# Performance work log

Hardware: AMD Instinct MI355X
Metric: run time of the kernel (lower is better)

## Reference

```python
import jax, jax.numpy as jnp
import numpy as np

B, TOPN, OUT, PAD, IOU_TH, IM = 16, 4, 224, 224, 0.25, 448
HP = IM + 2 * PAD  # padded image side = 896

_ANCHOR_SETTINGS = (
    dict(stride=32, size=48, scale=[2 ** (1. / 3.), 2 ** (2. / 3.)], aspect_ratio=[0.667, 1, 1.5]),
    dict(stride=64, size=96, scale=[2 ** (1. / 3.), 2 ** (2. / 3.)], aspect_ratio=[0.667, 1, 1.5]),
    dict(stride=128, size=192, scale=[1, 2 ** (1. / 3.), 2 ** (2. / 3.)], aspect_ratio=[0.667, 1, 1.5]),
)

def _edge_anchors(input_shape=(IM, IM)):
    # NTS-Net generate_default_anchor_maps: per layer, loop scale then aspect,
    # each emitting an HxW map flattened row-major -> matches tidy conv channel-major flatten.
    out = []
    for a in _ANCHOR_SETTINGS:
        st = a['stride']
        H = int(np.ceil(input_shape[0] / st)); W = int(np.ceil(input_shape[1] / st))
        cy = np.broadcast_to((np.arange(H) * st + st / 2.)[:, None], (H, W))
        cx = np.broadcast_to((np.arange(W) * st + st / 2.)[None, :], (H, W))
        for sc in a['scale']:
            for ar in a['aspect_ratio']:
                h = a['size'] * sc / np.sqrt(ar); w = a['size'] * sc * np.sqrt(ar)
                out.append(np.stack([cy - h / 2., cx - w / 2., cy + h / 2., cx + w / 2.], -1).reshape(-1, 4))
    e = np.concatenate(out, 0)
    return (e + PAD).astype(np.int32)  # module does (edge_anchors + 224).astype(int)


def _conv(x, w, b, stride, pad):
    y = jax.lax.conv_general_dilated(x, w, (stride, stride), [(pad, pad), (pad, pad)],
                                     dimension_numbers=('NCHW', 'OIHW', 'NCHW'))
    return y + b[None, :, None, None]


def _proposal_scores(rpn, w1, b1, w2, b2, w3, b3, wt1, bt1, wt2, bt2, wt3, bt3):
    d1 = jax.nn.relu(_conv(rpn, w1, b1, 1, 1))   # [B,128,14,14]
    d2 = jax.nn.relu(_conv(d1, w2, b2, 2, 1))    # [B,128,7,7]
    d3 = jax.nn.relu(_conv(d2, w3, b3, 2, 1))    # [B,128,4,4]
    bsz = rpn.shape[0]
    t1 = _conv(d1, wt1, bt1, 1, 0).reshape(bsz, -1)  # [B,1176]
    t2 = _conv(d2, wt2, bt2, 1, 0).reshape(bsz, -1)  # [B,294]
    t3 = _conv(d3, wt3, bt3, 1, 0).reshape(bsz, -1)  # [B,144]
    return jnp.concatenate([t1, t2, t3], axis=1)     # [B,1614]


def _nms_topn(scores, boxes, areas):
    # greedy hard NMS, fixed TOPN picks, suppress iou >= IOU_TH (matches upstream hard_nms)
    def step(s, _):
        i = jnp.argmax(s)
        sb = boxes[i]
        iy = jnp.clip(jnp.minimum(boxes[:, 2], sb[2]) - jnp.maximum(boxes[:, 0], sb[0]), 0.)
        ix = jnp.clip(jnp.minimum(boxes[:, 3], sb[3]) - jnp.maximum(boxes[:, 1], sb[1]), 0.)
        inter = iy * ix
        iou = inter / (areas + areas[i] - inter)
        return jnp.where(iou >= IOU_TH, -jnp.inf, s), i
    _, idxs = jax.lax.scan(step, scores, None, length=TOPN)
    return idxs  # [TOPN] int


def _crop_resize(x, anchors, top_idx):
    # batched replacement of the per-(i,j) F.interpolate(x_pad[i,:,y0:y1,x0:x1], 224, bilinear, align_corners=True)
    x_pad = jnp.pad(x, ((0, 0), (0, 0), (PAD, PAD), (PAD, PAD)))
    xp = jnp.transpose(x_pad, (0, 2, 3, 1))            # [B,HP,HP,3]
    bxs = anchors[top_idx].astype(jnp.float32)          # [B,T,4] (y0,x0,y1,x1)
    y0, x0, y1, x1 = bxs[..., 0], bxs[..., 1], bxs[..., 2], bxs[..., 3]
    t = jnp.arange(OUT, dtype=jnp.float32) / (OUT - 1)  # align_corners=True grid
    ys = y0[..., None] + t * (y1 - y0 - 1.)[..., None]  # [B,T,S] src rows in padded img
    xs = x0[..., None] + t * (x1 - x0 - 1.)[..., None]
    yi0 = jnp.floor(ys).astype(jnp.int32); yi1 = jnp.minimum(yi0 + 1, HP - 1)
    xi0 = jnp.floor(xs).astype(jnp.int32); xi1 = jnp.minimum(xi0 + 1, HP - 1)
    wy = (ys - yi0)[..., :, None, None]                 # [B,T,S,1,1]
    wx = (xs - xi0)[..., None, :, None]                 # [B,T,1,S,1]
    b = jnp.arange(x.shape[0])[:, None, None, None]
    g = lambda yi, xi: xp[b, yi[..., :, None], xi[..., None, :]]  # [B,T,S,S,3]
    v = (g(yi0, xi0) * (1 - wy) * (1 - wx) + g(yi0, xi1) * (1 - wy) * wx
         + g(yi1, xi0) * wy * (1 - wx) + g(yi1, xi1) * wy * wx)
    return jnp.transpose(v, (0, 1, 4, 2, 3))            # [B,T,3,S,S]


def setup_inputs() -> dict:
    key = jax.random.key(0)
    ks = jax.random.split(key, 16)
    he = lambda k, shape, fan: jax.random.normal(k, shape, jnp.float32) * np.sqrt(2.0 / fan)
    inp = {
        'x': jax.random.normal(ks[0], (B, 3, IM, IM), jnp.float32),
        'rpn_feature': jax.random.uniform(ks[1], (B, 2048, 14, 14), jnp.float32),
        'w_down1': he(ks[2], (128, 2048, 3, 3), 2048 * 9), 'b_down1': jnp.zeros((128,), jnp.float32),
        'w_down2': he(ks[3], (128, 128, 3, 3), 128 * 9),   'b_down2': jnp.zeros((128,), jnp.float32),
        'w_down3': he(ks[4], (128, 128, 3, 3), 128 * 9),   'b_down3': jnp.zeros((128,), jnp.float32),
        'w_tidy1': he(ks[5], (6, 128, 1, 1), 128),         'b_tidy1': jnp.zeros((6,), jnp.float32),
        'w_tidy2': he(ks[6], (6, 128, 1, 1), 128),         'b_tidy2': jnp.zeros((6,), jnp.float32),
        'w_tidy3': he(ks[7], (9, 128, 1, 1), 128),         'b_tidy3': jnp.zeros((9,), jnp.float32),
        'anchors': jnp.asarray(_edge_anchors(), jnp.int32),  # [1614,4]
    }
    return inp


def reference(x, rpn_feature, w_down1, b_down1, w_down2, b_down2, w_down3, b_down3,
              w_tidy1, b_tidy1, w_tidy2, b_tidy2, w_tidy3, b_tidy3, anchors):
    rpn_score = _proposal_scores(rpn_feature, w_down1, b_down1, w_down2, b_down2, w_down3, b_down3,
                                 w_tidy1, b_tidy1, w_tidy2, b_tidy2, w_tidy3, b_tidy3)
    boxes = anchors.astype(jnp.float32)
    areas = (boxes[:, 2] - boxes[:, 0]) * (boxes[:, 3] - boxes[:, 1])
    top_idx = jax.vmap(lambda s: _nms_topn(s, boxes, areas))(rpn_score)       # [B,TOPN]
    top_prob = jnp.take_along_axis(rpn_score, top_idx, axis=1)                # [B,TOPN]
    part_imgs = _crop_resize(x, anchors, top_idx).reshape(B * TOPN, 3, OUT, OUT)
    return part_imgs, top_idx, top_prob, rpn_score
```

## Files before the change

kernel.cpp:

```cpp
#include <hip/hip_runtime.h>
#include <math.h>

#define BATCH 16
#define TOPN 4
#define OUTS 224
#define PADW 224
#define IM 448
#define HP 896
#define NA 1614
#define IC1 2048
#define C128 128

#define N_PART (BATCH*TOPN*3*OUTS*OUTS)
#define OFF_TOPIDX  (N_PART)
#define OFF_TOPPROB (N_PART + BATCH*TOPN)
#define OFF_SCORE   (N_PART + 2*BATCH*TOPN)

#define WS_D1 0
#define WS_IDX (BATCH*C128*196)
#define WS_WT  (WS_IDX + 64)
#define NWT1 (9*2048*128)
#define NWT2 (9*128*128)
#define NIMG (16*32*16384)

typedef __attribute__((ext_vector_type(8))) short frag8;
typedef __attribute__((ext_vector_type(16))) float acc16;
typedef __attribute__((ext_vector_type(4)))  float acc4;

__device__ __forceinline__ unsigned short f2bf(float f) {
    unsigned int u = __float_as_uint(f);
    u = (u + 0x7fffu + ((u >> 16) & 1u)) >> 16;
    return (unsigned short)u;
}
__device__ __forceinline__ float bf2f(unsigned short h) {
    return __uint_as_float(((unsigned int)h) << 16);
}
__device__ __forceinline__ void cvt4(const float* v, ushort4* h, ushort4* lo) {
    unsigned short hh[4], ll[4];
#pragma unroll
    for (int e = 0; e < 4; ++e) { hh[e] = f2bf(v[e]); ll[e] = f2bf(v[e] - bf2f(hh[e])); }
    *h  = make_ushort4(hh[0], hh[1], hh[2], hh[3]);
    *lo = make_ushort4(ll[0], ll[1], ll[2], ll[3]);
}

__device__ __forceinline__ void wrepack_body(const float* __restrict__ w,
                                             unsigned short* __restrict__ w_hi,
                                             unsigned short* __restrict__ w_lo,
                                             int IC, int i) {
    if (i >= 128 * IC) return;
    int oc = i / IC, ic = i % IC;
    const float* src = w + (size_t)(oc * IC + ic) * 9;
#pragma unroll
    for (int tap = 0; tap < 9; ++tap) {
        float v = src[tap];
        unsigned short h = f2bf(v);
        size_t gi = ((size_t)tap * 128 + oc) * IC + ic;
        w_hi[gi] = h;
        w_lo[gi] = f2bf(v - bf2f(h));
    }
}

__device__ __forceinline__ void w1frag_body(const float* __restrict__ w1,
                                            unsigned short* __restrict__ w1h,
                                            unsigned short* __restrict__ w1l,
                                            int i) {
    if (i >= 32768) return;
    int oc5 = i & 31;
    int q8  = (i >> 5) & 1;
    int ot  = (i >> 6) & 3;
    int c   = (i >> 8) & 3;
    int h   = (i >> 10) & 1;
    int kg  = (i >> 11) & 15;
    int oc  = ot * 32 + oc5;
    int ic0 = kg * 128 + h * 64 + c * 16 + q8 * 8;
    int l   = q8 * 32 + oc5;
    const float* src = w1 + ((size_t)oc * IC1 + ic0) * 9;
    size_t dbase = (size_t)kg * 16384 + h * 8192 + c * 2048 + ot * 512 + l * 8;
#pragma unroll
    for (int t = 0; t < 9; ++t) {
        frag8 hv, lv;
#pragma unroll
        for (int e = 0; e < 8; ++e) {
            float v = src[e * 9 + t];
            unsigned short hs = f2bf(v);
            hv[e] = (short)hs;
            lv[e] = (short)f2bf(v - bf2f(hs));
        }
        size_t dst = dbase + (size_t)t * 262144;
        *(frag8*)&w1h[dst] = hv;
        *(frag8*)&w1l[dst] = lv;
    }
}

__global__ __launch_bounds__(256) void k_prep(
    const float* __restrict__ w1, unsigned short* __restrict__ w1h, unsigned short* __restrict__ w1l,
    const float* __restrict__ w2, unsigned short* __restrict__ w2h, unsigned short* __restrict__ w2l,
    const float* __restrict__ w3, unsigned short* __restrict__ w3h, unsigned short* __restrict__ w3l,
    const float* __restrict__ rpn, unsigned short* __restrict__ imgH,
    const float* __restrict__ b1, float* __restrict__ d1) {
    __shared__ float tile[64 * 201];
    const int tid = threadIdx.x;
    const int blk = blockIdx.x;
    if (blk < 128) {
        w1frag_body(w1, w1h, w1l, blk * 256 + tid);
    } else if (blk < 192) {
        wrepack_body(w2, w2h, w2l, C128, (blk - 128) * 256 + tid);
    } else if (blk < 256) {
        wrepack_body(w3, w3h, w3l, C128, (blk - 192) * 256 + tid);
    } else if (blk < 768) {
        const int bb = blk - 256;
        const int b = bb & 15, icg = bb >> 4;
        const int ic0 = icg * 64;
        char* img = (char*)(imgH + (size_t)bb * 16384);
        for (int qq = tid; qq < 3136; qq += 256) {
            int icl = qq / 49, r = qq % 49, p = r * 4;
            const float4 v = *(const float4*)&rpn[(size_t)(b * IC1 + ic0 + icl) * 196 + p];
            tile[icl * 201 + p + 0] = v.x;
            tile[icl * 201 + p + 1] = v.y;
            tile[icl * 201 + p + 2] = v.z;
            tile[icl * 201 + p + 3] = v.w;
        }
        __syncthreads();
        for (int qq = tid; qq < 3136; qq += 256) {
            int px = qq >> 4, ic4 = (qq & 15) * 4;
            float vv[4];
            unsigned short hh[4];
#pragma unroll
            for (int e = 0; e < 4; ++e) { vv[e] = tile[(ic4 + e) * 201 + px]; hh[e] = f2bf(vv[e]); }
            int pos = (px / 14 + 1) * 16 + (px % 14 + 1);
            int byo = (pos * 128 + ic4 * 2) ^ ((pos & 7) << 4);
            *(ushort4*)(img + byo) = make_ushort4(hh[0], hh[1], hh[2], hh[3]);
        }
        for (int qq = tid; qq < 960; qq += 256) {
            int hp = qq >> 4, sub = qq & 15;
            int pos;
            if (hp < 16)      pos = hp;
            else if (hp < 32) pos = 240 + (hp - 16);
            else if (hp < 46) pos = (hp - 31) * 16;
            else              pos = (hp - 45) * 16 + 15;
            *(ushort4*)(img + pos * 128 + sub * 8) = make_ushort4(0, 0, 0, 0);
        }
    } else {
        int i = (blk - 768) * 256 + tid;
        int base = i * 4;
        float4 v;
        v.x = b1[(base + 0) & 127]; v.y = b1[(base + 1) & 127];
        v.z = b1[(base + 2) & 127]; v.w = b1[(base + 3) & 127];
        *(float4*)&d1[base] = v;
    }
}


#define LOADB(it, BH, BL) { \
    const int o_ = ((it) >> 2) * 262144 + ((it) & 3) * 2048; \
    BH = *(const frag8*)&WHb[o_]; BL = *(const frag8*)&WLb[o_]; }

#define DOMFMA(it, BH, BL) { \
    const int tap_ = (it) >> 2; \
    const int off_ = (tap_ / 3) * 16 + (tap_ % 3); \
    const int kb_ = ((it) & 3) * 32 + q * 16; \
    frag8 aH[4]; \
    _Pragma("unroll") \
    for (int mt_ = 0; mt_ < 4; ++mt_) { \
        const int p_ = posa[mt_] + off_; \
        const int by_ = (p_ * 128 + kb_) ^ ((p_ & 7) << 4); \
        aH[mt_] = *(const frag8*)((const char*)inH + by_); \
    } \
    _Pragma("unroll") \
    for (int mt_ = 0; mt_ < 4; ++mt_) { \
        acc[mt_] = __builtin_amdgcn_mfma_f32_32x32x16_bf16(aH[mt_], BH, acc[mt_], 0, 0, 0); \
        acc[mt_] = __builtin_amdgcn_mfma_f32_32x32x16_bf16(aH[mt_], BL, acc[mt_], 0, 0, 0); \
    } }

__global__ __launch_bounds__(512, 4) void k_conv1_mfma(const unsigned short* __restrict__ imgH,
                                                       const unsigned short* __restrict__ wfh,
                                                       const unsigned short* __restrict__ wfl,
                                                       float* __restrict__ d1) {
    __shared__ unsigned short inH[256 * 64];

    const int tid = threadIdx.x;
    const int blk = blockIdx.x;
    const int b = blk >> 5;
    const int icg = blk & 31;
    const int l = tid & 63, w = tid >> 6;
    const int ln = l & 31, q = l >> 5;
    const int mtw = w & 1, ntw = w >> 1;

    {
        const char* src = (const char*)(imgH + ((size_t)(icg * 16 + b)) * 16384);
        char* dst = (char*)inH;
#pragma unroll
        for (int k = 0; k < 4; ++k) {
            frag8 v = *(const frag8*)(src + tid * 16 + k * 8192);
            *(frag8*)(dst + tid * 16 + k * 8192) = v;
        }
    }

    acc16 acc[4];
#pragma unroll
    for (int mt = 0; mt < 4; ++mt)
#pragma unroll
        for (int r = 0; r < 16; ++r) acc[mt][r] = 0.f;

    int posa[4];
#pragma unroll
    for (int mt = 0; mt < 4; ++mt) {
        int px = mtw * 128 + mt * 32 + ln;
        posa[mt] = (px < 196) ? ((px / 14) * 16 + (px % 14)) : 0;
    }

    const unsigned short* WHb = wfh + (size_t)icg * 8192 + ntw * 512 + (size_t)l * 8;
    const unsigned short* WLb = wfl + (size_t)icg * 8192 + ntw * 512 + (size_t)l * 8;

    __syncthreads();

    frag8 b0H, b0L, b1H, b1L;
    LOADB(0, b0H, b0L);
#pragma unroll
    for (int i2 = 0; i2 < 18; ++i2) {
        LOADB(i2 * 2 + 1, b1H, b1L);
        DOMFMA(i2 * 2, b0H, b0L);
        if (i2 < 17) LOADB(i2 * 2 + 2, b0H, b0L);
        DOMFMA(i2 * 2 + 1, b1H, b1L);
    }

    {
        const int oc = ntw * 32 + ln;
#pragma unroll
        for (int mt = 0; mt < 4; ++mt) {
#pragma unroll
            for (int r = 0; r < 16; ++r) {
                int m = (r & 3) + 8 * (r >> 2) + 4 * q;
                int px = mtw * 128 + mt * 32 + m;
                if (px < 196)
                    atomicAdd(&d1[(size_t)(b * 196 + px) * 128 + oc], acc[mt][r]);
            }
        }
    }
}

__global__ __launch_bounds__(512, 1) void k_tail(
    const float* __restrict__ d1,
    const unsigned short* __restrict__ w2h, const unsigned short* __restrict__ w2l,
    const unsigned short* __restrict__ w3h, const unsigned short* __restrict__ w3l,
    const float* __restrict__ b2, const float* __restrict__ b3,
    const float* __restrict__ wt1, const float* __restrict__ bt1,
    const float* __restrict__ wt2, const float* __restrict__ bt2,
    const float* __restrict__ wt3, const float* __restrict__ bt3,
    const int* __restrict__ anchors,
    float* __restrict__ score_out, float* __restrict__ out_idx,
    float* __restrict__ out_prob, int* __restrict__ idx_ws) {
    extern __shared__ char smem[];
    unsigned short* inH = (unsigned short*)(smem);
    unsigned short* inL = (unsigned short*)(smem + 43776);
    unsigned short* wHs = (unsigned short*)(smem + 87552);
    unsigned short* wLs = (unsigned short*)(smem + 105984);
    unsigned short* t1H = (unsigned short*)(smem + 124416);
    unsigned short* t1L = (unsigned short*)(smem + 126720);
    float*  d2f  = (float*)(smem + 129024);
    float*  sbuf = (float*)(smem + 154112);
    unsigned short* dhH = (unsigned short*)(smem);
    unsigned short* dhL = (unsigned short*)(smem + 27648);
    float*  d3f  = (float*)(smem + 55296);
    unsigned short* t2H = (unsigned short*)(smem + 63488);
    unsigned short* t2L = (unsigned short*)(smem + 65792);
    unsigned short* w3H = (unsigned short*)(smem + 68096);
    unsigned short* w3L = (unsigned short*)(smem + 86528);
    float* wt3s = (float*)(smem);
    float* y0s = (float*)(smem + 6464);
    float* x0s = (float*)(smem + 12928);
    float* y1s = (float*)(smem + 19392);
    float* x1s = (float*)(smem + 25856);
    float* ars = (float*)(smem + 32320);
    float* rv  = (float*)(smem + 38784);
    int*   ri  = (int*)(smem + 39808);

    const int tid = threadIdx.x;
    const int b = blockIdx.x;
    const int l = tid & 63, w = tid >> 6;
    const int ln = l & 31, q = l >> 5;
    const int l16 = l & 15, q4 = l >> 4;

    for (int i = tid; i < 304 * 72; i += 512) { inH[i] = 0; inL[i] = 0; }

    acc16 c2;
    acc4 t1a[2];
#pragma unroll
    for (int r = 0; r < 16; ++r) c2[r] = 0.f;
#pragma unroll
    for (int i = 0; i < 2; ++i)
#pragma unroll
        for (int r = 0; r < 4; ++r) t1a[i][r] = 0.f;

    const int mtw = w & 1, ntw = w >> 1;
    int posa2;
    {
        int px = mtw * 32 + ln;
        posa2 = (px < 49) ? ((px / 7) * 32 + (px % 7) * 2) : 256;
    }
    __syncthreads();

    for (int half = 0; half < 2; ++half) {
        const int ics = half * 64;
        for (int qq = tid; qq < 3136; qq += 512) {
            int px = qq >> 4, ic4 = (qq & 15) * 4;
            float4 v = *(const float4*)&d1[(size_t)(b * 196 + px) * 128 + ics + ic4];
            float vv[4] = {fmaxf(v.x, 0.f), fmaxf(v.y, 0.f), fmaxf(v.z, 0.f), fmaxf(v.w, 0.f)};
            ushort4 h4, l4; cvt4(vv, &h4, &l4);
            int pos = (px / 14 + 1) * 16 + (px % 14 + 1);
            *(ushort4*)&inH[pos * 72 + ic4] = h4;
            *(ushort4*)&inL[pos * 72 + ic4] = l4;
        }
        for (int qq = tid; qq < 1024; qq += 512) {
            int m = qq >> 6, k = qq & 63;
            float v = (m < 6) ? wt1[m * 128 + ics + k] : 0.f;
            unsigned short h = f2bf(v);
            t1H[m * 72 + k] = h;
            t1L[m * 72 + k] = f2bf(v - bf2f(h));
        }
        ushort4 pwh[4], pwl[4];
#pragma unroll
        for (int it = 0; it < 4; ++it) {
            int qq = tid + it * 512;
            int oc = qq >> 4, ic4 = (qq & 15) * 4;
            size_t gi = ((size_t)(0 * 128 + oc)) * C128 + ics + ic4;
            pwh[it] = *(const ushort4*)&w2h[gi];
            pwl[it] = *(const ushort4*)&w2l[gi];
        }
        __syncthreads();

        for (int tap = 0; tap < 9; ++tap) {
#pragma unroll
            for (int it = 0; it < 4; ++it) {
                int qq = tid + it * 512;
                int oc = qq >> 4, ic4 = (qq & 15) * 4;
                *(ushort4*)&wHs[oc * 72 + ic4] = pwh[it];
                *(ushort4*)&wLs[oc * 72 + ic4] = pwl[it];
            }
            if (tap < 8) {
#pragma unroll
                for (int it = 0; it < 4; ++it) {
                    int qq = tid + it * 512;
                    int oc = qq >> 4, ic4 = (qq & 15) * 4;
                    size_t gi = ((size_t)((tap + 1) * 128 + oc)) * C128 + ics + ic4;
                    pwh[it] = *(const ushort4*)&w2h[gi];
                    pwl[it] = *(const ushort4*)&w2l[gi];
                }
            }
            __syncthreads();
            const int off = (tap / 3) * 16 + (tap % 3);
#pragma unroll
            for (int c = 0; c < 4; ++c) {
                const int ko = c * 16 + q * 8;
                int pp = (posa2 + off) * 72 + ko;
                frag8 aH = *(const frag8*)&inH[pp];
                frag8 aL = *(const frag8*)&inL[pp];
                int oc = ntw * 32 + ln;
                frag8 bH = *(const frag8*)&wHs[oc * 72 + ko];
                frag8 bL = *(const frag8*)&wLs[oc * 72 + ko];
                c2 = __builtin_amdgcn_mfma_f32_32x32x16_bf16(aH, bH, c2, 0, 0, 0);
                c2 = __builtin_amdgcn_mfma_f32_32x32x16_bf16(aH, bL, c2, 0, 0, 0);
                c2 = __builtin_amdgcn_mfma_f32_32x32x16_bf16(aL, bH, c2, 0, 0, 0);
            }
            __syncthreads();
        }

#pragma unroll
        for (int i = 0; i < 2; ++i) {
            int px = (w * 2 + i) * 16 + l16;
            int pos = (px < 196) ? ((px / 14 + 1) * 16 + (px % 14 + 1)) : 256;
#pragma unroll
            for (int c = 0; c < 2; ++c) {
                int ko = c * 32 + q4 * 8;
                frag8 aH = *(const frag8*)&t1H[l16 * 72 + ko];
                frag8 aL = *(const frag8*)&t1L[l16 * 72 + ko];
                frag8 bH = *(const frag8*)&inH[pos * 72 + ko];
                frag8 bL = *(const frag8*)&inL[pos * 72 + ko];
                t1a[i] = __builtin_amdgcn_mfma_f32_16x16x32_bf16(aH, bH, t1a[i], 0, 0, 0);
                t1a[i] = __builtin_amdgcn_mfma_f32_16x16x32_bf16(aH, bL, t1a[i], 0, 0, 0);
                t1a[i] = __builtin_amdgcn_mfma_f32_16x16x32_bf16(aL, bH, t1a[i], 0, 0, 0);
            }
        }
        __syncthreads();
    }

    {
        int oc = ntw * 32 + ln;
        float bias = b2[oc];
#pragma unroll
        for (int r = 0; r < 16; ++r) {
            int m = (r & 3) + 8 * (r >> 2) + 4 * q;
            int px = mtw * 32 + m;
            if (px < 49) d2f[px * 128 + oc] = fmaxf(c2[r] + bias, 0.f);
        }
    }
#pragma unroll
    for (int i = 0; i < 2; ++i) {
        int px = (w * 2 + i) * 16 + l16;
#pragma unroll
        for (int r = 0; r < 4; ++r) {
            int oc = q4 * 4 + r;
            if (oc < 6 && px < 196) {
                float v = t1a[i][r] + bt1[oc];
                sbuf[oc * 196 + px] = v;
                score_out[b * NA + oc * 196 + px] = v;
            }
        }
    }
    __syncthreads();

    for (int i = tid; i < 192 * 72; i += 512) { dhH[i] = 0; dhL[i] = 0; }

    acc16 c3;
    acc4 t2a;
#pragma unroll
    for (int r = 0; r < 16; ++r) c3[r] = 0.f;
#pragma unroll
    for (int r = 0; r < 4; ++r) t2a[r] = 0.f;

    const int posb3 = (ln < 16) ? ((ln / 4) * 32 + (ln % 4) * 2) : 144;
    const int pxt2 = (w - 4) * 16 + l16;
    const int posbt2 = (w >= 4 && pxt2 < 49) ? ((pxt2 / 7 + 1) * 16 + (pxt2 % 7 + 1)) : 144;
    __syncthreads();

    for (int half = 0; half < 2; ++half) {
        const int ics = half * 64;
        for (int qq = tid; qq < 784; qq += 512) {
            int px = qq >> 4, ic4 = (qq & 15) * 4;
            float4 v = *(const float4*)&d2f[px * 128 + ics + ic4];
            float vv[4] = {v.x, v.y, v.z, v.w};
            ushort4 h4, l4; cvt4(vv, &h4, &l4);
            int pos = (px / 7 + 1) * 16 + (px % 7 + 1);
            *(ushort4*)&dhH[pos * 72 + ic4] = h4;
            *(ushort4*)&dhL[pos * 72 + ic4] = l4;
        }
        for (int qq = tid; qq < 1024; qq += 512) {
            int m = qq >> 6, k = qq & 63;
            float v = (m < 6) ? wt2[m * 128 + ics + k] : 0.f;
            unsigned short h = f2bf(v);
            t2H[m * 72 + k] = h;
            t2L[m * 72 + k] = f2bf(v - bf2f(h));
        }
        ushort4 pwh[4], pwl[4];
#pragma unroll
        for (int it = 0; it < 4; ++it) {
            int qq = tid + it * 512;
            int oc = qq >> 4, ic4 = (qq & 15) * 4;
            size_t gi = ((size_t)(0 * 128 + oc)) * C128 + ics + ic4;
            pwh[it] = *(const ushort4*)&w3h[gi];
            pwl[it] = *(const ushort4*)&w3l[gi];
        }
        __syncthreads();

        for (int tap = 0; tap < 9; ++tap) {
#pragma unroll
            for (int it = 0; it < 4; ++it) {
                int qq = tid + it * 512;
                int oc = qq >> 4, ic4 = (qq & 15) * 4;
                *(ushort4*)&w3H[oc * 72 + ic4] = pwh[it];
                *(ushort4*)&w3L[oc * 72 + ic4] = pwl[it];
            }
            if (tap < 8) {
#pragma unroll
                for (int it = 0; it < 4; ++it) {
                    int qq = tid + it * 512;
                    int oc = qq >> 4, ic4 = (qq & 15) * 4;
                    size_t gi = ((size_t)((tap + 1) * 128 + oc)) * C128 + ics + ic4;
                    pwh[it] = *(const ushort4*)&w3h[gi];
                    pwl[it] = *(const ushort4*)&w3l[gi];
                }
            }
            __syncthreads();
            const int off = (tap / 3) * 16 + (tap % 3);
            if (w < 4) {
#pragma unroll
                for (int c = 0; c < 4; ++c) {
                    const int ko = c * 16 + q * 8;
                    int pp = (posb3 + off) * 72 + ko;
                    frag8 aH = *(const frag8*)&dhH[pp];
                    frag8 aL = *(const frag8*)&dhL[pp];
                    int oc = w * 32 + ln;
                    frag8 bH = *(const frag8*)&w3H[oc * 72 + ko];
                    frag8 bL = *(const frag8*)&w3L[oc * 72 + ko];
                    c3 = __builtin_amdgcn_mfma_f32_32x32x16_bf16(aH, bH, c3, 0, 0, 0);
                    c3 = __builtin_amdgcn_mfma_f32_32x32x16_bf16(aH, bL, c3, 0, 0, 0);
                    c3 = __builtin_amdgcn_mfma_f32_32x32x16_bf16(aL, bH, c3, 0, 0, 0);
                }
            } else if (tap == 0) {
#pragma unroll
                for (int c = 0; c < 2; ++c) {
                    int ko = c * 32 + q4 * 8;
                    frag8 aH = *(const frag8*)&t2H[l16 * 72 + ko];
                    frag8 aL = *(const frag8*)&t2L[l16 * 72 + ko];
                    frag8 bH = *(const frag8*)&dhH[posbt2 * 72 + ko];
                    frag8 bL = *(const frag8*)&dhL[posbt2 * 72 + ko];
                    t2a = __builtin_amdgcn_mfma_f32_16x16x32_bf16(aH, bH, t2a, 0, 0, 0);
                    t2a = __builtin_amdgcn_mfma_f32_16x16x32_bf16(aH, bL, t2a, 0, 0, 0);
                    t2a = __builtin_amdgcn_mfma_f32_16x16x32_bf16(aL, bH, t2a, 0, 0, 0);
                }
            }
            __syncthreads();
        }
    }

    if (w < 4) {
        int oc = w * 32 + ln;
        float bias = b3[oc];
#pragma unroll
        for (int r = 0; r < 16; ++r) {
            int px = (r & 3) + 8 * (r >> 2) + 4 * q;
            if (px < 16) d3f[oc * 16 + px] = fmaxf(c3[r] + bias, 0.f);
        }
    } else {
#pragma unroll
        for (int r = 0; r < 4; ++r) {
            int oc = q4 * 4 + r;
            if (oc < 6 && pxt2 < 49) {
                float v = t2a[r] + bt2[oc];
                sbuf[1176 + oc * 49 + pxt2] = v;
                score_out[b * NA + 1176 + oc * 49 + pxt2] = v;
            }
        }
    }
    for (int i = tid; i < 1152; i += 512) wt3s[i] = wt3[i];
    __syncthreads();

    if (tid < 144) {
        int oc = tid >> 4, px = tid & 15;
        float s = bt3[oc];
        for (int ic = 0; ic < 128; ++ic) s += wt3s[oc * 128 + ic] * d3f[ic * 16 + px];
        sbuf[1470 + oc * 16 + px] = s;
        score_out[b * NA + 1470 + oc * 16 + px] = s;
    }
    for (int j = tid; j < NA; j += 512) {
        int4 a = ((const int4*)anchors)[j];
        float a0 = (float)a.x, a1 = (float)a.y, a2 = (float)a.z, a3 = (float)a.w;
        y0s[j] = a0; x0s[j] = a1; y1s[j] = a2; x1s[j] = a3;
        ars[j] = (a2 - a0) * (a3 - a1);
    }
    __syncthreads();

    for (int it = 0; it < TOPN; ++it) {
        float bv = -INFINITY; int bi = NA;
        for (int j = tid; j < NA; j += 512) {
            float v = sbuf[j];
            if (v > bv || (v == bv && j < bi)) { bv = v; bi = j; }
        }
#pragma unroll
        for (int d = 1; d < 64; d <<= 1) {
            float ov = __shfl_xor(bv, d, 64);
            int   oi = __shfl_xor(bi, d, 64);
            if (ov > bv || (ov == bv && oi < bi)) { bv = ov; bi = oi; }
        }
        if (l == 0) { rv[w] = bv; ri[w] = bi; }
        __syncthreads();
        if (tid == 0) {
            float V = rv[0]; int K = ri[0];
#pragma unroll
            for (int j = 1; j < 8; ++j) {
                float ov = rv[j]; int oi = ri[j];
                if (ov > V || (ov == V && oi < K)) { V = ov; K = oi; }
            }
            ri[8] = K;
            out_idx[b * TOPN + it] = (float)K;
            out_prob[b * TOPN + it] = V;
            idx_ws[b * TOPN + it] = K;
        }
        __syncthreads();
        int K = ri[8];
        float ky0 = y0s[K], kx0 = x0s[K], ky1 = y1s[K], kx1 = x1s[K], ka = ars[K];
        for (int j = tid; j < NA; j += 512) {
            float iy = fmaxf(fminf(y1s[j], ky1) - fmaxf(y0s[j], ky0), 0.f);
            float ix = fmaxf(fminf(x1s[j], kx1) - fmaxf(x0s[j], kx0), 0.f);
            float inter = iy * ix;
            float iou = inter / (ars[j] + ka - inter);
            if (iou >= 0.25f) sbuf[j] = -INFINITY;
        }
        __syncthreads();
    }
}

__global__ __launch_bounds__(256) void k_crop(const float* __restrict__ x,
                                              const int* __restrict__ anchors,
                                              const int* __restrict__ idx_ws,
                                              float* __restrict__ out) {
    int blk = blockIdx.x;
    int crop = blk / OUTS;
    int i = blk % OUTS;
    int j = threadIdx.x;
    if (j >= OUTS) return;
    int b = crop >> 2;
    int a = idx_ws[crop];
    int y0 = anchors[a * 4], x0 = anchors[a * 4 + 1];
    int y1 = anchors[a * 4 + 2], x1 = anchors[a * 4 + 3];

    float ti = (float)i / 223.f;
    float ys = (float)y0 + ti * (float)(y1 - y0 - 1);
    int yi0 = (int)ys;
    int yi1 = min(yi0 + 1, HP - 1);
    float wy = ys - (float)yi0;

    float tj = (float)j / 223.f;
    float xs = (float)x0 + tj * (float)(x1 - x0 - 1);
    int xi0 = (int)xs;
    int xi1 = min(xi0 + 1, HP - 1);
    float wx = xs - (float)xi0;

    int ry0 = yi0 - PADW, ry1 = yi1 - PADW, rx0 = xi0 - PADW, rx1 = xi1 - PADW;
    bool vy0 = (ry0 >= 0) && (ry0 < IM), vy1 = (ry1 >= 0) && (ry1 < IM);
    bool vx0 = (rx0 >= 0) && (rx0 < IM), vx1 = (rx1 >= 0) && (rx1 < IM);

    float w00 = (1.f - wy) * (1.f - wx), w01 = (1.f - wy) * wx;
    float w10 = wy * (1.f - wx), w11 = wy * wx;

#pragma unroll
    for (int c = 0; c < 3; ++c) {
        const float* xp = x + (size_t)(b * 3 + c) * IM * IM;
        float g00 = (vy0 && vx0) ? xp[ry0 * IM + rx0] : 0.f;
        float g01 = (vy0 && vx1) ? xp[ry0 * IM + rx1] : 0.f;
        float g10 = (vy1 && vx0) ? xp[ry1 * IM + rx0] : 0.f;
        float g11 = (vy1 && vx1) ? xp[ry1 * IM + rx1] : 0.f;
        out[(size_t)(crop * 3 + c) * OUTS * OUTS + i * OUTS + j] =
            g00 * w00 + g01 * w01 + g10 * w10 + g11 * w11;
    }
}

extern "C" void kernel_launch(void* const* d_in, const int* in_sizes, int n_in,
                              void* d_out, int out_size, void* d_ws, size_t ws_size,
                              hipStream_t stream) {
    (void)in_sizes; (void)n_in; (void)out_size; (void)ws_size;
    const float* x    = (const float*)d_in[0];
    const float* rpn  = (const float*)d_in[1];
    const float* w1   = (const float*)d_in[2];
    const float* b1   = (const float*)d_in[3];
    const float* w2   = (const float*)d_in[4];
    const float* b2   = (const float*)d_in[5];
    const float* w3   = (const float*)d_in[6];
    const float* b3   = (const float*)d_in[7];
    const float* wt1  = (const float*)d_in[8];
    const float* bt1  = (const float*)d_in[9];
    const float* wt2  = (const float*)d_in[10];
    const float* bt2  = (const float*)d_in[11];
    const float* wt3  = (const float*)d_in[12];
    const float* bt3  = (const float*)d_in[13];
    const int*   anc  = (const int*)d_in[14];

    float* out = (float*)d_out;
    float* ws  = (float*)d_ws;
    float* d1  = ws + WS_D1;
    int*   idxw = (int*)(ws + WS_IDX);
    unsigned short* w1h = (unsigned short*)(ws + WS_WT);
    unsigned short* w1l = w1h + NWT1;
    unsigned short* w2h = w1l + NWT1;
    unsigned short* w2l = w2h + NWT2;
    unsigned short* w3h = w2l + NWT2;
    unsigned short* w3l = w3h + NWT2;
    unsigned short* imgH = w3l + NWT2;

    static const int TAIL_LDS = 160568;
    hipFuncSetAttribute((const void*)k_tail, hipFuncAttributeMaxDynamicSharedMemorySize, TAIL_LDS);

    k_prep<<<1160, 256, 0, stream>>>(w1, w1h, w1l, w2, w2h, w2l, w3, w3h, w3l,
                                     rpn, imgH, b1, d1);
    k_conv1_mfma<<<512, 512, 0, stream>>>(imgH, w1h, w1l, d1);
    k_tail<<<BATCH, 512, TAIL_LDS, stream>>>(d1, w2h, w2l, w3h, w3l, b2, b3,
                                             wt1, bt1, wt2, bt2, wt3, bt3, anc,
                                             out + OFF_SCORE, out + OFF_TOPIDX,
                                             out + OFF_TOPPROB, idxw);
    k_crop<<<BATCH * TOPN * OUTS, 256, 0, stream>>>(x, anc, idxw, out);
}
```

Measured before the change: 273.9 us.

## Load conv2/conv3 weights as pre-packed MFMA fragments directly from global memory

Repacks the conv2 and conv3 weights into MFMA B-fragment layout during the prep kernel. The tail kernel now reads these fragments straight from global memory into registers with a 4-deep prefetch pipeline, instead of staging each tap through LDS with two block barriers per tap. This removes 18 syncthreads and the LDS weight traffic per conv stage, at the cost of more register pressure and exposed global load latency. The conv1 B-operand prefetch also goes from double to triple buffering.

```diff
diff --git a/kernel.cpp b/kernel.cpp
--- a/kernel.cpp
+++ b/kernel.cpp
@@ -41,23 +41,6 @@
     for (int e = 0; e < 4; ++e) { hh[e] = f2bf(v[e]); ll[e] = f2bf(v[e] - bf2f(hh[e])); }
     *h  = make_ushort4(hh[0], hh[1], hh[2], hh[3]);
     *lo = make_ushort4(ll[0], ll[1], ll[2], ll[3]);
-}
-
-__device__ __forceinline__ void wrepack_body(const float* __restrict__ w,
-                                             unsigned short* __restrict__ w_hi,
-                                             unsigned short* __restrict__ w_lo,
-                                             int IC, int i) {
-    if (i >= 128 * IC) return;
-    int oc = i / IC, ic = i % IC;
-    const float* src = w + (size_t)(oc * IC + ic) * 9;
-#pragma unroll
-    for (int tap = 0; tap < 9; ++tap) {
-        float v = src[tap];
-        unsigned short h = f2bf(v);
-        size_t gi = ((size_t)tap * 128 + oc) * IC + ic;
-        w_hi[gi] = h;
-        w_lo[gi] = f2bf(v - bf2f(h));
-    }
 }
 
 __device__ __forceinline__ void w1frag_body(const float* __restrict__ w1,
@@ -92,10 +75,41 @@
     }
 }
 
+__device__ __forceinline__ void wfrag128_body(const float* __restrict__ w,
+                                              unsigned short* __restrict__ wh,
+                                              unsigned short* __restrict__ wl,
+                                              int i) {
+    if (i >= 16384) return;
+    int oc5 = i & 31;
+    int q8  = (i >> 5) & 1;
+    int ot  = (i >> 6) & 3;
+    int c   = (i >> 8) & 3;
+    int h   = (i >> 10) & 1;
+    int oc  = ot * 32 + oc5;
+    int ic0 = h * 64 + c * 16 + q8 * 8;
+    int l   = q8 * 32 + oc5;
+    const float* src = w + ((size_t)oc * C128 + ic0) * 9;
+    size_t dbase = (size_t)h * 8192 + c * 2048 + ot * 512 + l * 8;
+#pragma unroll
+    for (int t = 0; t < 9; ++t) {
+        frag8 hv, lv;
+#pragma unroll
+        for (int e = 0; e < 8; ++e) {
+            float v = src[e * 9 + t];
+            unsigned short hs = f2bf(v);
+            hv[e] = (short)hs;
+            lv[e] = (short)f2bf(v - bf2f(hs));
+        }
+        size_t dst = dbase + (size_t)t * 16384;
+        *(frag8*)&wh[dst] = hv;
+        *(frag8*)&wl[dst] = lv;
+    }
+}
+
 __global__ __launch_bounds__(256) void k_prep(
     const float* __restrict__ w1, unsigned short* __restrict__ w1h, unsigned short* __restrict__ w1l,
-    const float* __restrict__ w2, unsigned short* __restrict__ w2h, unsigned short* __restrict__ w2l,
-    const float* __restrict__ w3, unsigned short* __restrict__ w3h, unsigned short* __restrict__ w3l,
+    const float* __restrict__ w2, unsigned short* __restrict__ w2fh, unsigned short* __restrict__ w2fl,
+    const float* __restrict__ w3, unsigned short* __restrict__ w3fh, unsigned short* __restrict__ w3fl,
     const float* __restrict__ rpn, unsigned short* __restrict__ imgH,
     const float* __restrict__ b1, float* __restrict__ d1) {
     __shared__ float tile[64 * 201];
@@ -104,9 +118,9 @@
     if (blk < 128) {
         w1frag_body(w1, w1h, w1l, blk * 256 + tid);
     } else if (blk < 192) {
-        wrepack_body(w2, w2h, w2l, C128, (blk - 128) * 256 + tid);
+        wfrag128_body(w2, w2fh, w2fl, (blk - 128) * 256 + tid);
     } else if (blk < 256) {
-        wrepack_body(w3, w3h, w3l, C128, (blk - 192) * 256 + tid);
+        wfrag128_body(w3, w3fh, w3fl, (blk - 192) * 256 + tid);
     } else if (blk < 768) {
         const int bb = blk - 256;
         const int b = bb & 15, icg = bb >> 4;
@@ -214,14 +228,15 @@
 
     __syncthreads();
 
-    frag8 b0H, b0L, b1H, b1L;
-    LOADB(0, b0H, b0L);
-#pragma unroll
-    for (int i2 = 0; i2 < 18; ++i2) {
-        LOADB(i2 * 2 + 1, b1H, b1L);
-        DOMFMA(i2 * 2, b0H, b0L);
-        if (i2 < 17) LOADB(i2 * 2 + 2, b0H, b0L);
-        DOMFMA(i2 * 2 + 1, b1H, b1L);
+    frag8 B0H, B0L, B1H, B1L, B2H, B2L;
+    LOADB(0, B0H, B0L);
+    LOADB(1, B1H, B1L);
+    LOADB(2, B2H, B2L);
+#pragma unroll
+    for (int g = 0; g < 12; ++g) {
+        DOMFMA(g * 3 + 0, B0H, B0L); if (g < 11) LOADB(g * 3 + 3, B0H, B0L);
+        DOMFMA(g * 3 + 1, B1H, B1L); if (g < 11) LOADB(g * 3 + 4, B1H, B1L);
+        DOMFMA(g * 3 + 2, B2H, B2L); if (g < 11) LOADB(g * 3 + 5, B2H, B2L);
     }
 
     {
@@ -239,10 +254,41 @@
     }
 }
 
+
+#define LOADB2(it, BH, BL) { \
+    const int o_ = ((it) >> 2) * 16384 + ((it) & 3) * 2048; \
+    BH = *(const frag8*)&W2H[o_]; BL = *(const frag8*)&W2L[o_]; }
+
+#define DOC2(it, BH, BL) { \
+    const int tap_ = (it) >> 2; \
+    const int off_ = (tap_ / 3) * 16 + (tap_ % 3); \
+    const int ko_ = ((it) & 3) * 16 + q * 8; \
+    const int pp_ = (posa2 + off_) * 72 + ko_; \
+    frag8 aH = *(const frag8*)&inH[pp_]; \
+    frag8 aL = *(const frag8*)&inL[pp_]; \
+    c2 = __builtin_amdgcn_mfma_f32_32x32x16_bf16(aH, BH, c2, 0, 0, 0); \
+    c2 = __builtin_amdgcn_mfma_f32_32x32x16_bf16(aH, BL, c2, 0, 0, 0); \
+    c2 = __builtin_amdgcn_mfma_f32_32x32x16_bf16(aL, BH, c2, 0, 0, 0); }
+
+#define LOADB3(it, BH, BL) { \
+    const int o_ = ((it) >> 2) * 16384 + ((it) & 3) * 2048; \
+    BH = *(const frag8*)&W3Hp[o_]; BL = *(const frag8*)&W3Lp[o_]; }
+
+#define DOC3(it, BH, BL) { \
+    const int tap_ = (it) >> 2; \
+    const int off_ = (tap_ / 3) * 16 + (tap_ % 3); \
+    const int ko_ = ((it) & 3) * 16 + q * 8; \
+    const int pp_ = (posb3 + off_) * 72 + ko_; \
+    frag8 aH = *(const frag8*)&dhH[pp_]; \
+    frag8 aL = *(const frag8*)&dhL[pp_]; \
+    c3 = __builtin_amdgcn_mfma_f32_32x32x16_bf16(aH, BH, c3, 0, 0, 0); \
+    c3 = __builtin_amdgcn_mfma_f32_32x32x16_bf16(aH, BL, c3, 0, 0, 0); \
+    c3 = __builtin_amdgcn_mfma_f32_32x32x16_bf16(aL, BH, c3, 0, 0, 0); }
+
 __global__ __launch_bounds__(512, 1) void k_tail(
     const float* __restrict__ d1,
-    const unsigned short* __restrict__ w2h, const unsigned short* __restrict__ w2l,
-    const unsigned short* __restrict__ w3h, const unsigned short* __restrict__ w3l,
+    const unsigned short* __restrict__ w2fh, const unsigned short* __restrict__ w2fl,
+    const unsigned short* __restrict__ w3fh, const unsigned short* __restrict__ w3fl,
     const float* __restrict__ b2, const float* __restrict__ b3,
     const float* __restrict__ wt1, const float* __restrict__ bt1,
     const float* __restrict__ wt2, const float* __restrict__ bt2,
@@ -253,8 +299,6 @@
     extern __shared__ char smem[];
     unsigned short* inH = (unsigned short*)(smem);
     unsigned short* inL = (unsigned short*)(smem + 43776);
-    unsigned short* wHs = (unsigned short*)(smem + 87552);
-    unsigned short* wLs = (unsigned short*)(smem + 105984);
     unsigned short* t1H = (unsigned short*)(smem + 124416);
     unsigned short* t1L = (unsigned short*)(smem + 126720);
     float*  d2f  = (float*)(smem + 129024);
@@ -264,8 +308,6 @@
     float*  d3f  = (float*)(smem + 55296);
     unsigned short* t2H = (unsigned short*)(smem + 63488);
     unsigned short* t2L = (unsigned short*)(smem + 65792);
-    unsigned short* w3H = (unsigned short*)(smem + 68096);
-    unsigned short* w3L = (unsigned short*)(smem + 86528);
     float* wt3s = (float*)(smem);
     float* y0s = (float*)(smem + 6464);
     float* x0s = (float*)(smem + 12928);
@@ -318,51 +360,23 @@
             t1H[m * 72 + k] = h;
             t1L[m * 72 + k] = f2bf(v - bf2f(h));
         }
-        ushort4 pwh[4], pwl[4];
-#pragma unroll
-        for (int it = 0; it < 4; ++it) {
-            int qq = tid + it * 512;
-            int oc = qq >> 4, ic4 = (qq & 15) * 4;
-            size_t gi = ((size_t)(0 * 128 + oc)) * C128 + ics + ic4;
-            pwh[it] = *(const ushort4*)&w2h[gi];
-            pwl[it] = *(const ushort4*)&w2l[gi];
-        }
-        __syncthreads();
-
-        for (int tap = 0; tap < 9; ++tap) {
-#pragma unroll
-            for (int it = 0; it < 4; ++it) {
-                int qq = tid + it * 512;
-                int oc = qq >> 4, ic4 = (qq & 15) * 4;
-                *(ushort4*)&wHs[oc * 72 + ic4] = pwh[it];
-                *(ushort4*)&wLs[oc * 72 + ic4] = pwl[it];
-            }
-            if (tap < 8) {
-#pragma unroll
-                for (int it = 0; it < 4; ++it) {
-                    int qq = tid + it * 512;
-                    int oc = qq >> 4, ic4 = (qq & 15) * 4;
-                    size_t gi = ((size_t)((tap + 1) * 128 + oc)) * C128 + ics + ic4;
-                    pwh[it] = *(const ushort4*)&w2h[gi];
-                    pwl[it] = *(const ushort4*)&w2l[gi];
-                }
-            }
-            __syncthreads();
-            const int off = (tap / 3) * 16 + (tap % 3);
-#pragma unroll
-            for (int c = 0; c < 4; ++c) {
-                const int ko = c * 16 + q * 8;
-                int pp = (posa2 + off) * 72 + ko;
-                frag8 aH = *(const frag8*)&inH[pp];
-                frag8 aL = *(const frag8*)&inL[pp];
-                int oc = ntw * 32 + ln;
-                frag8 bH = *(const frag8*)&wHs[oc * 72 + ko];
-                frag8 bL = *(const frag8*)&wLs[oc * 72 + ko];
-                c2 = __builtin_amdgcn_mfma_f32_32x32x16_bf16(aH, bH, c2, 0, 0, 0);
-                c2 = __builtin_amdgcn_mfma_f32_32x32x16_bf16(aH, bL, c2, 0, 0, 0);
-                c2 = __builtin_amdgcn_mfma_f32_32x32x16_bf16(aL, bH, c2, 0, 0, 0);
-            }
-            __syncthreads();
+        __syncthreads();
+
+        {
+            const unsigned short* W2H = w2fh + half * 8192 + ntw * 512 + (size_t)l * 8;
+            const unsigned short* W2L = w2fl + half * 8192 + ntw * 512 + (size_t)l * 8;
+            frag8 B0H, B0L, B1H, B1L, B2H, B2L, B3H, B3L;
+            LOADB2(0, B0H, B0L);
+            LOADB2(1, B1H, B1L);
+            LOADB2(2, B2H, B2L);
+            LOADB2(3, B3H, B3L);
+#pragma unroll
+            for (int g = 0; g < 9; ++g) {
+                DOC2(g * 4 + 0, B0H, B0L); if (g < 8) LOADB2(g * 4 + 4, B0H, B0L);
+                DOC2(g * 4 + 1, B1H, B1L); if (g < 8) LOADB2(g * 4 + 5, B1H, B1L);
+                DOC2(g * 4 + 2, B2H, B2L); if (g < 8) LOADB2(g * 4 + 6, B2H, B2L);
+                DOC2(g * 4 + 3, B3H, B3L); if (g < 8) LOADB2(g * 4 + 7, B3H, B3L);
+            }
         }
 
 #pragma unroll
@@ -441,66 +455,37 @@
             t2H[m * 72 + k] = h;
             t2L[m * 72 + k] = f2bf(v - bf2f(h));
         }
-        ushort4 pwh[4], pwl[4];
-#pragma unroll
-        for (int it = 0; it < 4; ++it) {
-            int qq = tid + it * 512;
-            int oc = qq >> 4, ic4 = (qq & 15) * 4;
-            size_t gi = ((size_t)(0 * 128 + oc)) * C128 + ics + ic4;
-            pwh[it] = *(const ushort4*)&w3h[gi];
-            pwl[it] = *(const ushort4*)&w3l[gi];
-        }
-        __syncthreads();
-
-        for (int tap = 0; tap < 9; ++tap) {
-#pragma unroll
-            for (int it = 0; it < 4; ++it) {
-                int qq = tid + it * 512;
-                int oc = qq >> 4, ic4 = (qq & 15) * 4;
-                *(ushort4*)&w3H[oc * 72 + ic4] = pwh[it];
-                *(ushort4*)&w3L[oc * 72 + ic4] = pwl[it];
-            }
-            if (tap < 8) {
-#pragma unroll
-                for (int it = 0; it < 4; ++it) {
-                    int qq = tid + it * 512;
-                    int oc = qq >> 4, ic4 = (qq & 15) * 4;
-                    size_t gi = ((size_t)((tap + 1) * 128 + oc)) * C128 + ics + ic4;
-                    pwh[it] = *(const ushort4*)&w3h[gi];
-                    pwl[it] = *(const ushort4*)&w3l[gi];
-                }
-            }
-            __syncthreads();
-            const int off = (tap / 3) * 16 + (tap % 3);
-            if (w < 4) {
-#pragma unroll
-                for (int c = 0; c < 4; ++c) {
-                    const int ko = c * 16 + q * 8;
-                    int pp = (posb3 + off) * 72 + ko;
-                    frag8 aH = *(const frag8*)&dhH[pp];
-                    frag8 aL = *(const frag8*)&dhL[pp];
-                    int oc = w * 32 + ln;
-                    frag8 bH = *(const frag8*)&w3H[oc * 72 + ko];
-                    frag8 bL = *(const frag8*)&w3L[oc * 72 + ko];
-                    c3 = __builtin_amdgcn_mfma_f32_32x32x16_bf16(aH, bH, c3, 0, 0, 0);
-                    c3 = __builtin_amdgcn_mfma_f32_32x32x16_bf16(aH, bL, c3, 0, 0, 0);
-                    c3 = __builtin_amdgcn_mfma_f32_32x32x16_bf16(aL, bH, c3, 0, 0, 0);
-                }
-            } else if (tap == 0) {
-#pragma unroll
-                for (int c = 0; c < 2; ++c) {
-                    int ko = c * 32 + q4 * 8;
-                    frag8 aH = *(const frag8*)&t2H[l16 * 72 + ko];
-                    frag8 aL = *(const frag8*)&t2L[l16 * 72 + ko];
-                    frag8 bH = *(const frag8*)&dhH[posbt2 * 72 + ko];
-                    frag8 bL = *(const frag8*)&dhL[posbt2 * 72 + ko];
-                    t2a = __builtin_amdgcn_mfma_f32_16x16x32_bf16(aH, bH, t2a, 0, 0, 0);
-                    t2a = __builtin_amdgcn_mfma_f32_16x16x32_bf16(aH, bL, t2a, 0, 0, 0);
-                    t2a = __builtin_amdgcn_mfma_f32_16x16x32_bf16(aL, bH, t2a, 0, 0, 0);
-                }
-            }
-            __syncthreads();
-        }
+        __syncthreads();
+
+        if (w < 4) {
+            const unsigned short* W3Hp = w3fh + half * 8192 + w * 512 + (size_t)l * 8;
+            const unsigned short* W3Lp = w3fl + half * 8192 + w * 512 + (size_t)l * 8;
+            frag8 B0H, B0L, B1H, B1L, B2H, B2L, B3H, B3L;
+            LOADB3(0, B0H, B0L);
+            LOADB3(1, B1H, B1L);
+            LOADB3(2, B2H, B2L);
+            LOADB3(3, B3H, B3L);
+#pragma unroll
+            for (int g = 0; g < 9; ++g) {
+                DOC3(g * 4 + 0, B0H, B0L); if (g < 8) LOADB3(g * 4 + 4, B0H, B0L);
+                DOC3(g * 4 + 1, B1H, B1L); if (g < 8) LOADB3(g * 4 + 5, B1H, B1L);
+                DOC3(g * 4 + 2, B2H, B2L); if (g < 8) LOADB3(g * 4 + 6, B2H, B2L);
+                DOC3(g * 4 + 3, B3H, B3L); if (g < 8) LOADB3(g * 4 + 7, B3H, B3L);
+            }
+        } else {
+#pragma unroll
+            for (int c = 0; c < 2; ++c) {
+                int ko = c * 32 + q4 * 8;
+                frag8 aH = *(const frag8*)&t2H[l16 * 72 + ko];
+                frag8 aL = *(const frag8*)&t2L[l16 * 72 + ko];
+                frag8 bH = *(const frag8*)&dhH[posbt2 * 72 + ko];
+                frag8 bL = *(const frag8*)&dhL[posbt2 * 72 + ko];
+                t2a = __builtin_amdgcn_mfma_f32_16x16x32_bf16(aH, bH, t2a, 0, 0, 0);
+                t2a = __builtin_amdgcn_mfma_f32_16x16x32_bf16(aH, bL, t2a, 0, 0, 0);
+                t2a = __builtin_amdgcn_mfma_f32_16x16x32_bf16(aL, bH, t2a, 0, 0, 0);
+            }
+        }
+        __syncthreads();
     }
 
     if (w < 4) {
@@ -651,19 +636,19 @@
     int*   idxw = (int*)(ws + WS_IDX);
     unsigned short* w1h = (unsigned short*)(ws + WS_WT);
     unsigned short* w1l = w1h + NWT1;
-    unsigned short* w2h = w1l + NWT1;
-    unsigned short* w2l = w2h + NWT2;
-    unsigned short* w3h = w2l + NWT2;
-    unsigned short* w3l = w3h + NWT2;
-    unsigned short* imgH = w3l + NWT2;
+    unsigned short* w2fh = w1l + NWT1;
+    unsigned short* w2fl = w2fh + NWT2;
+    unsigned short* w3fh = w2fl + NWT2;
+    unsigned short* w3fl = w3fh + NWT2;
+    unsigned short* imgH = w3fl + NWT2;
 
     static const int TAIL_LDS = 160568;
     hipFuncSetAttribute((const void*)k_tail, hipFuncAttributeMaxDynamicSharedMemorySize, TAIL_LDS);
 
-    k_prep<<<1160, 256, 0, stream>>>(w1, w1h, w1l, w2, w2h, w2l, w3, w3h, w3l,
+    k_prep<<<1160, 256, 0, stream>>>(w1, w1h, w1l, w2, w2fh, w2fl, w3, w3fh, w3fl,
                                      rpn, imgH, b1, d1);
     k_conv1_mfma<<<512, 512, 0, stream>>>(imgH, w1h, w1l, d1);
-    k_tail<<<BATCH, 512, TAIL_LDS, stream>>>(d1, w2h, w2l, w3h, w3l, b2, b3,
+    k_tail<<<BATCH, 512, TAIL_LDS, stream>>>(d1, w2fh, w2fl, w3fh, w3fl, b2, b3,
                                              wt1, bt1, wt2, bt2, wt3, bt3, anc,
                                              out + OFF_SCORE, out + OFF_TOPIDX,
                                              out + OFF_TOPPROB, idxw);
```

Result: no change. 272.3 us (-0.6%).
